# Kernel tuning notes

Hardware: AMD Instinct MI355X
Metric: run time of the kernel (lower is better)

Reference implementation:

```python
import jax, jax.numpy as jnp
import numpy as np

B, N, C = 128, 320, 768
H = 12
T = 64    # template tokens (8x8)
S = 256   # search tokens (16x16)


def setup_inputs() -> dict:
    key = jax.random.key(0)
    k1, k2, k3, k4 = jax.random.split(key, 4)
    return {
        "x1": jax.random.normal(k1, (B, N, C), dtype=jnp.float32),
        "x2": jax.random.normal(k2, (B, N, C), dtype=jnp.float32),
        "qkv_w": jax.random.normal(k3, (3 * C, C), dtype=jnp.float32) * 0.02,
        "proj_w": jax.random.normal(k4, (C, C), dtype=jnp.float32) * 0.02,
        "proj_b": jnp.zeros((C,), dtype=jnp.float32),
    }


def reference(x1, x2, qkv_w, proj_w, proj_b):
    # concat template tokens from x1 with search tokens from x2
    x = jnp.concatenate([x1[:, :T, :], x2[:, T:, :]], axis=1)  # [B, N, C]
    b, n, c = x.shape
    d = c // H
    scale = d ** -0.5

    qkv = (x @ qkv_w.T).reshape(b, n, 3, H, d).transpose(2, 0, 3, 1, 4)  # [3,B,H,N,D]
    q, k, v = qkv[0], qkv[1], qkv[2]

    # template -> template self-attention
    q_mt, k_mt, v_mt = q[:, :, :T], k[:, :, :T], v[:, :, :T]
    attn_mt = jax.nn.softmax(jnp.einsum('bhtd,bhsd->bhts', q_mt, k_mt) * scale, axis=-1)
    x_mt = jnp.einsum('bhts,bhsd->bhtd', attn_mt, v_mt).transpose(0, 2, 1, 3).reshape(b, T, c)

    # search -> all cross+self attention
    q_s = q[:, :, T:]
    attn_s = jax.nn.softmax(jnp.einsum('bhqd,bhkd->bhqk', q_s, k) * scale, axis=-1)
    x_s = jnp.einsum('bhqk,bhkd->bhqd', attn_s, v).transpose(0, 2, 1, 3).reshape(b, S, c)

    out = jnp.concatenate([x_mt, x_s], axis=1) @ proj_w.T + proj_b
    return out
```

## Files before the change

kernel.cpp:

```cpp
#include <hip/hip_runtime.h>
#include <hip/hip_bf16.h>
#include <stdint.h>

#define B_   128
#define N_   320
#define C_   768
#define H_   12
#define D_   64
#define NT_  (B_*N_)
#define K3_  (3*C_)
#define NKT  12
#define TE   (256*64)

typedef __attribute__((ext_vector_type(8))) __bf16 bf16x8;
typedef __attribute__((ext_vector_type(4))) float  f32x4;

__device__ __forceinline__ unsigned short f2bf(float f) {
  union { float f; unsigned u; } v; v.f = f;
  return (unsigned short)((v.u + 0x7fffu + ((v.u >> 16) & 1u)) >> 16);
}

__device__ __forceinline__ void gload16(const unsigned short* g, unsigned short* l) {
  __builtin_amdgcn_global_load_lds((const __attribute__((address_space(1))) void*)g,
                                   (__attribute__((address_space(3))) void*)l,
                                   16, 0, 0);
}

__global__ void prep_x(const float* __restrict__ x1, const float* __restrict__ x2,
                       unsigned short* __restrict__ xb) {
  const unsigned total4 = (unsigned)NT_ * C_ / 4;
  const unsigned stride = gridDim.x * blockDim.x;
  for (unsigned i = blockIdx.x * blockDim.x + threadIdx.x; i < total4; i += stride) {
    unsigned tok = i / (C_ / 4);
    unsigned n   = tok % N_;
    const float* src = (n < 64u) ? x1 : x2;
    float4 v = *(const float4*)(src + (size_t)i * 4u);
    ushort4 o;
    o.x = f2bf(v.x); o.y = f2bf(v.y); o.z = f2bf(v.z); o.w = f2bf(v.w);
    *(ushort4*)(xb + (size_t)i * 4u) = o;
  }
}

__global__ void prep_w(const float* __restrict__ qkv_w, const float* __restrict__ proj_w,
                       unsigned short* __restrict__ wq, unsigned short* __restrict__ wp) {
  const int QKV4 = (K3_ * C_) / 4;
  const int Q4   = (C_ * C_) / 4;
  const int P4   = (C_ * C_) / 4;
  int i = blockIdx.x * 256 + threadIdx.x;
  if (i < QKV4) {
    float s = (i < Q4) ? 0.125f : 1.0f;
    float4 v = *(const float4*)(qkv_w + (size_t)i * 4);
    ushort4 o;
    o.x = f2bf(v.x * s); o.y = f2bf(v.y * s); o.z = f2bf(v.z * s); o.w = f2bf(v.w * s);
    *(ushort4*)(wq + (size_t)i * 4) = o;
  } else if (i < QKV4 + P4) {
    int j = i - QKV4;
    float4 v = *(const float4*)(proj_w + (size_t)j * 4);
    ushort4 o;
    o.x = f2bf(v.x); o.y = f2bf(v.y); o.z = f2bf(v.z); o.w = f2bf(v.w);
    *(ushort4*)(wp + (size_t)j * 4) = o;
  }
}

__device__ __forceinline__ void stage_half(const unsigned short* __restrict__ g,
                                           int grow0, int kt,
                                           unsigned short* lds_tile, int half,
                                           int w, int lane) {
  const int r0 = half * 128 + w * 16;
  const int rr = lane >> 3;
  const int sp = (lane & 7) ^ rr;
#pragma unroll
  for (int i = 0; i < 2; i++) {
    const unsigned short* gp = g + (size_t)(grow0 + r0 + i * 8 + rr) * 768 + kt * 64 + sp * 8;
    unsigned short* lp = lds_tile + (r0 + i * 8) * 64;
    gload16(gp, lp);
  }
}

__device__ __forceinline__ bf16x8 lds_frag(const unsigned short* tile, int row, int pp) {
  const char* p = (const char*)tile + row * 128 + (((pp) ^ (row & 7)) * 16);
  return *(const bf16x8*)p;
}

__device__ __forceinline__ void gemm_kloop(const unsigned short* __restrict__ Ag,
                                           const unsigned short* __restrict__ Wg,
                                           int row0, int col0,
                                           unsigned short* As, unsigned short* Bs,
                                           f32x4 (&acc)[8][4]) {
  const int tid = threadIdx.x, lane = tid & 63, w = tid >> 6;
  const int wr = w >> 2, wc = w & 3;
  const int lr = lane & 15, kg = lane >> 4;

  stage_half(Ag, row0, 0, As, 0, w, lane);
  stage_half(Ag, row0, 0, As, 1, w, lane);
  stage_half(Wg, col0, 0, Bs, 0, w, lane);
  stage_half(Wg, col0, 0, Bs, 1, w, lane);
  stage_half(Wg, col0, 1, Bs + TE, 0, w, lane);
  stage_half(Wg, col0, 1, Bs + TE, 1, w, lane);
  asm volatile("s_waitcnt vmcnt(4)" ::: "memory");
  __builtin_amdgcn_s_barrier();
  asm volatile("" ::: "memory");

  bf16x8 bf_[2][4];
#pragma unroll 2
  for (int t = 0; t < NKT; ++t) {
    unsigned short* Ac = As + (t & 1) * TE;
    unsigned short* Bc = Bs + (t & 1) * TE;
#pragma unroll
    for (int q = 0; q < 4; ++q) {
      bf16x8 af_[2][2];
#pragma unroll
      for (int f = 0; f < 2; ++f)
#pragma unroll
        for (int ks = 0; ks < 2; ++ks)
          af_[f][ks] = lds_frag(Ac, wr * 128 + q * 32 + f * 16 + lr, ks * 4 + kg);
      if (q == 0) {
#pragma unroll
        for (int nf = 0; nf < 4; ++nf)
#pragma unroll
          for (int ks = 0; ks < 2; ++ks)
            bf_[ks][nf] = lds_frag(Bc, wc * 64 + nf * 16 + lr, ks * 4 + kg);
      }
      if (q == 0)      { if (t + 1 < NKT) stage_half(Ag, row0, t + 1, As + ((t + 1) & 1) * TE, 0, w, lane); }
      else if (q == 1) { if (t + 1 < NKT) stage_half(Ag, row0, t + 1, As + ((t + 1) & 1) * TE, 1, w, lane); }
      else if (q == 2) { if (t + 2 < NKT) stage_half(Wg, col0, t + 2, Bs + (t & 1) * TE, 0, w, lane); }
      else             { if (t + 2 < NKT) stage_half(Wg, col0, t + 2, Bs + (t & 1) * TE, 1, w, lane); }
      asm volatile("" ::: "memory");
      __builtin_amdgcn_s_barrier();
      asm volatile("" ::: "memory");
      __builtin_amdgcn_s_setprio(1);
#pragma unroll
      for (int f = 0; f < 2; ++f)
#pragma unroll
        for (int nf = 0; nf < 4; ++nf) {
          const int mf = q * 2 + f;
          acc[mf][nf] = __builtin_amdgcn_mfma_f32_16x16x32_bf16(af_[f][0], bf_[0][nf], acc[mf][nf], 0, 0, 0);
          acc[mf][nf] = __builtin_amdgcn_mfma_f32_16x16x32_bf16(af_[f][1], bf_[1][nf], acc[mf][nf], 0, 0, 0);
        }
      __builtin_amdgcn_s_setprio(0);
      asm volatile("" ::: "memory");
      if (q == 3) {
        if (t < NKT - 2)       asm volatile("s_waitcnt vmcnt(4)" ::: "memory");
        else if (t == NKT - 2) asm volatile("s_waitcnt vmcnt(0)" ::: "memory");
      }
      __builtin_amdgcn_s_barrier();
      asm volatile("" ::: "memory");
    }
  }
}

__global__ void __launch_bounds__(512, 2) gemm_qkv(const unsigned short* __restrict__ A,
                                                   const unsigned short* __restrict__ W,
                                                   unsigned short* __restrict__ qb,
                                                   unsigned short* __restrict__ kb,
                                                   unsigned short* __restrict__ vb) {
  __shared__ __align__(16) unsigned short As[2 * TE];
  __shared__ __align__(16) unsigned short Bs[2 * TE];
  const int tid = threadIdx.x, lane = tid & 63, w = tid >> 6;
  const int wr = w >> 2, wc = w & 3;
  const int lr = lane & 15, kg = lane >> 4;
  const int bid = blockIdx.x;
  const int wg = (bid & 7) * 180 + (bid >> 3);
  const int bm = wg / 9, bn = wg % 9;
  const int row0 = bm * 256, col0 = bn * 256;

  f32x4 acc[8][4] = {};
  gemm_kloop(A, W, row0, col0, As, Bs, acc);

  const int which = bn / 3;
  const int colq  = (bn % 3) * 256 + wc * 64;
  if (which == 2) {
#pragma unroll
    for (int mf = 0; mf < 8; ++mf) {
      const int m0 = row0 + wr * 128 + mf * 16 + kg * 4;
      const unsigned bq = (unsigned)m0 / 320u;
      const unsigned t0 = (unsigned)m0 - bq * 320u;
#pragma unroll
      for (int nf = 0; nf < 4; ++nf) {
        const int nn = colq + nf * 16 + lr;
        const int h = nn >> 6, dd = nn & 63;
        ushort4 o;
        o.x = f2bf(acc[mf][nf][0]); o.y = f2bf(acc[mf][nf][1]);
        o.z = f2bf(acc[mf][nf][2]); o.w = f2bf(acc[mf][nf][3]);
        *(ushort4*)&vb[(((int)bq * 12 + h) * 64 + dd) * 320 + (int)t0] = o;
      }
    }
  } else {
    unsigned short* dst = (which == 0) ? qb : kb;
#pragma unroll
    for (int mf = 0; mf < 8; ++mf) {
      const int m0 = row0 + wr * 128 + mf * 16 + kg * 4;
      const unsigned bq = (unsigned)m0 / 320u;
      const unsigned t0 = (unsigned)m0 - bq * 320u;
#pragma unroll
      for (int nf = 0; nf < 4; ++nf) {
        const int nn = colq + nf * 16 + lr;
        const int h = nn >> 6, dd = nn & 63;
        const int base = (((int)bq * 12 + h) * 320 + (int)t0) * 64 + dd;
#pragma unroll
        for (int r = 0; r < 4; r++)
          dst[base + r * 64] = f2bf(acc[mf][nf][r]);
      }
    }
  }
}

__global__ void __launch_bounds__(256) attn(const unsigned short* __restrict__ qb,
                                            const unsigned short* __restrict__ kb,
                                            const unsigned short* __restrict__ vb,
                                            unsigned short* __restrict__ ab) {
  __shared__ __align__(16) unsigned short Ks[64 * 64];
  __shared__ __align__(16) unsigned short Vt[64 * 64];
  __shared__ __align__(16) unsigned short Pl[4 * 16 * 64];
  const int bid = blockIdx.x;
  const int qt = bid % 5, bh = bid / 5;
  const int tid = threadIdx.x, lane = tid & 63, w = tid >> 6;
  const int lr = lane & 15, kg = lane >> 4;

  const int qrow = qt * 64 + w * 16 + lr;
  const unsigned short* qptr = qb + (bh * 320 + qrow) * 64;
  const bf16x8 qa0 = *(const bf16x8*)(qptr + kg * 8);
  const bf16x8 qa1 = *(const bf16x8*)(qptr + 32 + kg * 8);

  f32x4 o[4] = {};
  float mrun[4] = {-1e30f, -1e30f, -1e30f, -1e30f};
  float lrun[4] = {0.f, 0.f, 0.f, 0.f};
  const int nchunk = (qt == 0) ? 1 : 5;

  const int c0 = w, c1 = w + 4;
  const int srow0 = c0 * 8 + (lane >> 3);
  const int srow1 = c1 * 8 + (lane >> 3);
  const int slot  = lane & 7;
  const int part0 = slot ^ (srow0 & 7);
  const int part1 = slot ^ (srow1 & 7);
  const unsigned short* kbase = kb + bh * 320 * 64;
  const unsigned short* vbase = vb + bh * 64 * 320;
  unsigned short* lk0 = &Ks[c0 * 512];
  unsigned short* lk1 = &Ks[c1 * 512];
  unsigned short* lv0 = &Vt[c0 * 512];
  unsigned short* lv1 = &Vt[c1 * 512];
  char* PwB = (char*)&Pl[w * 1024];

  for (int kc = 0; kc < nchunk; kc++) {
    gload16(kbase + (kc * 64 + srow0) * 64 + part0 * 8, lk0);
    gload16(kbase + (kc * 64 + srow1) * 64 + part1 * 8, lk1);
    gload16(vbase + srow0 * 320 + kc * 64 + part0 * 8, lv0);
    gload16(vbase + srow1 * 320 + kc * 64 + part1 * 8, lv1);
    __syncthreads();

    f32x4 s[4];
#pragma unroll
    for (int kt = 0; kt < 4; kt++) {
      const int key = kt * 16 + lr;
      const char* kr = (const char*)Ks + key * 128;
      const unsigned sw = (unsigned)((key & 7) << 4);
      bf16x8 k0 = *(const bf16x8*)(kr + ((kg * 16) ^ sw));
      bf16x8 k1 = *(const bf16x8*)(kr + ((64 + kg * 16) ^ sw));
      f32x4 z = {0.f, 0.f, 0.f, 0.f};
      z = __builtin_amdgcn_mfma_f32_16x16x32_bf16(qa0, k0, z, 0, 0, 0);
      z = __builtin_amdgcn_mfma_f32_16x16x32_bf16(qa1, k1, z, 0, 0, 0);
      s[kt] = z;
    }

#pragma unroll
    for (int r = 0; r < 4; r++) {
      float rm = fmaxf(fmaxf(s[0][r], s[1][r]), fmaxf(s[2][r], s[3][r]));
      rm = fmaxf(rm, __shfl_xor(rm, 1));
      rm = fmaxf(rm, __shfl_xor(rm, 2));
      rm = fmaxf(rm, __shfl_xor(rm, 4));
      rm = fmaxf(rm, __shfl_xor(rm, 8));
      const float mn = fmaxf(mrun[r], rm);
      const float alpha = __expf(mrun[r] - mn);
      mrun[r] = mn;
      const int q = kg * 4 + r;
      char* prow = PwB + q * 128;
      const unsigned sw = (unsigned)((q & 7) << 4);
      float rs = 0.f;
#pragma unroll
      for (int kt = 0; kt < 4; kt++) {
        const float p = __expf(s[kt][r] - mn);
        rs += p;
        const int key = kt * 16 + lr;
        *(unsigned short*)(prow + ((key * 2) ^ sw)) = f2bf(p);
      }
      rs += __shfl_xor(rs, 1);
      rs += __shfl_xor(rs, 2);
      rs += __shfl_xor(rs, 4);
      rs += __shfl_xor(rs, 8);
      lrun[r] = lrun[r] * alpha + rs;
#pragma unroll
      for (int dt = 0; dt < 4; dt++) o[dt][r] *= alpha;
    }

    asm volatile("s_waitcnt lgkmcnt(0)" ::: "memory");

    {
      const char* par = (const char*)PwB + lr * 128;
      const unsigned swp = (unsigned)((lr & 7) << 4);
      bf16x8 p0 = *(const bf16x8*)(par + ((kg * 16) ^ swp));
      bf16x8 p1 = *(const bf16x8*)(par + ((64 + kg * 16) ^ swp));
#pragma unroll
      for (int dt = 0; dt < 4; dt++) {
        const int d = dt * 16 + lr;
        const char* vr = (const char*)Vt + d * 128;
        const unsigned swv = (unsigned)((d & 7) << 4);
        bf16x8 v0 = *(const bf16x8*)(vr + ((kg * 16) ^ swv));
        bf16x8 v1 = *(const bf16x8*)(vr + ((64 + kg * 16) ^ swv));
        o[dt] = __builtin_amdgcn_mfma_f32_16x16x32_bf16(p0, v0, o[dt], 0, 0, 0);
        o[dt] = __builtin_amdgcn_mfma_f32_16x16x32_bf16(p1, v1, o[dt], 0, 0, 0);
      }
    }
    __syncthreads();
  }

  const int b = bh / 12, h = bh - b * 12;
#pragma unroll
  for (int r = 0; r < 4; r++) {
    const float inv = 1.0f / lrun[r];
    const int token = b * 320 + qt * 64 + w * 16 + kg * 4 + r;
    unsigned short* orow = ab + token * 768 + h * 64;
#pragma unroll
    for (int dt = 0; dt < 4; dt++)
      orow[dt * 16 + lr] = f2bf(o[dt][r] * inv);
  }
}

__global__ void __launch_bounds__(512, 2) gemm_proj(const unsigned short* __restrict__ A,
                                                    const unsigned short* __restrict__ W,
                                                    const float* __restrict__ bias,
                                                    float* __restrict__ out) {
  __shared__ __align__(16) unsigned short As[2 * TE];
  __shared__ __align__(16) unsigned short Bs[2 * TE];
  const int tid = threadIdx.x, lane = tid & 63, w = tid >> 6;
  const int wr = w >> 2, wc = w & 3;
  const int lr = lane & 15, kg = lane >> 4;
  const int bid = blockIdx.x;
  const int wg = (bid & 7) * 60 + (bid >> 3);
  const int bm = wg / 3, bn = wg % 3;
  const int row0 = bm * 256, col0 = bn * 256;

  f32x4 acc[8][4] = {};
  gemm_kloop(A, W, row0, col0, As, Bs, acc);

#pragma unroll
  for (int nf = 0; nf < 4; ++nf) {
    const int nn = col0 + wc * 64 + nf * 16 + lr;
    const float bv = bias[nn];
#pragma unroll
    for (int mf = 0; mf < 8; ++mf) {
      const int m0 = row0 + wr * 128 + mf * 16 + kg * 4;
      float* po = out + (size_t)m0 * 768 + nn;
#pragma unroll
      for (int r = 0; r < 4; r++)
        po[(size_t)r * 768] = acc[mf][nf][r] + bv;
    }
  }
}

extern "C" void kernel_launch(void* const* d_in, const int* in_sizes, int n_in,
                              void* d_out, int out_size, void* d_ws, size_t ws_size,
                              hipStream_t stream) {
  (void)in_sizes; (void)n_in; (void)out_size; (void)ws_size;
  const float* x1     = (const float*)d_in[0];
  const float* x2     = (const float*)d_in[1];
  const float* qkv_w  = (const float*)d_in[2];
  const float* proj_w = (const float*)d_in[3];
  const float* proj_b = (const float*)d_in[4];
  float* out = (float*)d_out;

  const size_t TOK = (size_t)NT_ * C_;
  unsigned short* xb = (unsigned short*)d_ws;
  unsigned short* qb = xb + TOK;
  unsigned short* kb = qb + TOK;
  unsigned short* vb = kb + TOK;
  unsigned short* ab = vb + TOK;
  unsigned short* wq = ab + TOK;
  unsigned short* wp = wq + (size_t)K3_ * C_;

  prep_x<<<8192, 256, 0, stream>>>(x1, x2, xb);
  prep_w<<<2304, 256, 0, stream>>>(qkv_w, proj_w, wq, wp);
  gemm_qkv<<<160 * 9, 512, 0, stream>>>(xb, wq, qb, kb, vb);
  attn<<<1536 * 5, 256, 0, stream>>>(qb, kb, vb, ab);
  gemm_proj<<<160 * 3, 512, 0, stream>>>(ab, wp, proj_b, out);
}
```

Baseline: 409.9 us.

## Rewrite GEMM k-loop as macro-unrolled pipeline with precomputed LDS/global pointers

```diff
diff --git a/kernel.cpp b/kernel.cpp
--- a/kernel.cpp
+++ b/kernel.cpp
@@ -62,91 +62,93 @@
   }
 }
 
-__device__ __forceinline__ void stage_half(const unsigned short* __restrict__ g,
-                                           int grow0, int kt,
-                                           unsigned short* lds_tile, int half,
-                                           int w, int lane) {
-  const int r0 = half * 128 + w * 16;
-  const int rr = lane >> 3;
-  const int sp = (lane & 7) ^ rr;
-#pragma unroll
-  for (int i = 0; i < 2; i++) {
-    const unsigned short* gp = g + (size_t)(grow0 + r0 + i * 8 + rr) * 768 + kt * 64 + sp * 8;
-    unsigned short* lp = lds_tile + (r0 + i * 8) * 64;
-    gload16(gp, lp);
-  }
-}
-
-__device__ __forceinline__ bf16x8 lds_frag(const unsigned short* tile, int row, int pp) {
-  const char* p = (const char*)tile + row * 128 + (((pp) ^ (row & 7)) * 16);
-  return *(const bf16x8*)p;
-}
-
-__device__ __forceinline__ void gemm_kloop(const unsigned short* __restrict__ Ag,
-                                           const unsigned short* __restrict__ Wg,
-                                           int row0, int col0,
-                                           unsigned short* As, unsigned short* Bs,
-                                           f32x4 (&acc)[8][4]) {
+#define BARR do { asm volatile("" ::: "memory"); __builtin_amdgcn_s_barrier(); asm volatile("" ::: "memory"); } while(0)
+#define DSW  asm volatile("s_waitcnt lgkmcnt(0)" ::: "memory")
+#define VMW(n) asm volatile("s_waitcnt vmcnt(" #n ")" ::: "memory")
+#define NOPW do {} while(0)
+#define PRIO1 __builtin_amdgcn_s_setprio(1)
+#define PRIO0 __builtin_amdgcn_s_setprio(0)
+#define RD(base, off) (*(const bf16x8*)((base) + (off)))
+
+#define LDA_Q(QQ, PARX) do { \
+    a_[0][0] = RD(bAk0, (PARX)*32768 + (QQ)*8192);        \
+    a_[0][1] = RD(bAk1, (PARX)*32768 + (QQ)*8192);        \
+    a_[1][0] = RD(bAk0, (PARX)*32768 + (QQ)*8192 + 2048); \
+    a_[1][1] = RD(bAk1, (PARX)*32768 + (QQ)*8192 + 2048); } while(0)
+
+#define LDB(PARX) do { \
+    _Pragma("unroll") for (int nf = 0; nf < 4; ++nf) { \
+      b_[0][nf] = RD(bBk0, (PARX)*32768 + nf*2048); \
+      b_[1][nf] = RD(bBk1, (PARX)*32768 + nf*2048); } } while(0)
+
+#define MFMA_Q(QQ) do { \
+    _Pragma("unroll") for (int ks = 0; ks < 2; ++ks) \
+    _Pragma("unroll") for (int f = 0; f < 2; ++f) \
+    _Pragma("unroll") for (int nf = 0; nf < 4; ++nf) \
+      acc[(QQ)*2+f][nf] = __builtin_amdgcn_mfma_f32_16x16x32_bf16(a_[f][ks], b_[ks][nf], acc[(QQ)*2+f][nf], 0, 0, 0); \
+  } while(0)
+
+#define STGA_H0(PARX) do { gload16(gA00, dA + ((PARX)^1)*TE);        gload16(gA01, dA + ((PARX)^1)*TE + 512);  gA00 += 64; gA01 += 64; } while(0)
+#define STGA_H1(PARX) do { gload16(gA10, dA + ((PARX)^1)*TE + 8192); gload16(gA11, dA + ((PARX)^1)*TE + 8704); gA10 += 64; gA11 += 64; } while(0)
+#define STGB_H0(PARX) do { gload16(gB00, dB + (PARX)*TE);            gload16(gB01, dB + (PARX)*TE + 512);      gB00 += 64; gB01 += 64; } while(0)
+#define STGB_H1(PARX) do { gload16(gB10, dB + (PARX)*TE + 8192);     gload16(gB11, dB + (PARX)*TE + 8704);     gB10 += 64; gB11 += 64; } while(0)
+
+#define KTILE(PARX, SA_, SB_, W1_, W3_) do { \
+    LDA_Q(0, PARX); LDB(PARX); if (SA_) STGA_H0(PARX); \
+    BARR; DSW; PRIO1; MFMA_Q(0); PRIO0; BARR; \
+    LDA_Q(1, PARX); if (SA_) STGA_H1(PARX); \
+    BARR; DSW; PRIO1; MFMA_Q(1); PRIO0; W1_; BARR; \
+    LDA_Q(2, PARX); if (SB_) STGB_H0(PARX); \
+    BARR; DSW; PRIO1; MFMA_Q(2); PRIO0; BARR; \
+    LDA_Q(3, PARX); if (SB_) STGB_H1(PARX); \
+    BARR; DSW; PRIO1; MFMA_Q(3); PRIO0; W3_; BARR; \
+  } while(0)
+
+__device__ __forceinline__ void kloop256(const unsigned short* __restrict__ Ag,
+                                         const unsigned short* __restrict__ Wg,
+                                         int row0, int col0,
+                                         unsigned short* As, unsigned short* Bs,
+                                         f32x4 (&acc)[8][4]) {
   const int tid = threadIdx.x, lane = tid & 63, w = tid >> 6;
   const int wr = w >> 2, wc = w & 3;
   const int lr = lane & 15, kg = lane >> 4;
-
-  stage_half(Ag, row0, 0, As, 0, w, lane);
-  stage_half(Ag, row0, 0, As, 1, w, lane);
-  stage_half(Wg, col0, 0, Bs, 0, w, lane);
-  stage_half(Wg, col0, 0, Bs, 1, w, lane);
-  stage_half(Wg, col0, 1, Bs + TE, 0, w, lane);
-  stage_half(Wg, col0, 1, Bs + TE, 1, w, lane);
-  asm volatile("s_waitcnt vmcnt(4)" ::: "memory");
-  __builtin_amdgcn_s_barrier();
-  asm volatile("" ::: "memory");
-
-  bf16x8 bf_[2][4];
-#pragma unroll 2
-  for (int t = 0; t < NKT; ++t) {
-    unsigned short* Ac = As + (t & 1) * TE;
-    unsigned short* Bc = Bs + (t & 1) * TE;
-#pragma unroll
-    for (int q = 0; q < 4; ++q) {
-      bf16x8 af_[2][2];
-#pragma unroll
-      for (int f = 0; f < 2; ++f)
-#pragma unroll
-        for (int ks = 0; ks < 2; ++ks)
-          af_[f][ks] = lds_frag(Ac, wr * 128 + q * 32 + f * 16 + lr, ks * 4 + kg);
-      if (q == 0) {
-#pragma unroll
-        for (int nf = 0; nf < 4; ++nf)
-#pragma unroll
-          for (int ks = 0; ks < 2; ++ks)
-            bf_[ks][nf] = lds_frag(Bc, wc * 64 + nf * 16 + lr, ks * 4 + kg);
-      }
-      if (q == 0)      { if (t + 1 < NKT) stage_half(Ag, row0, t + 1, As + ((t + 1) & 1) * TE, 0, w, lane); }
-      else if (q == 1) { if (t + 1 < NKT) stage_half(Ag, row0, t + 1, As + ((t + 1) & 1) * TE, 1, w, lane); }
-      else if (q == 2) { if (t + 2 < NKT) stage_half(Wg, col0, t + 2, Bs + (t & 1) * TE, 0, w, lane); }
-      else             { if (t + 2 < NKT) stage_half(Wg, col0, t + 2, Bs + (t & 1) * TE, 1, w, lane); }
-      asm volatile("" ::: "memory");
-      __builtin_amdgcn_s_barrier();
-      asm volatile("" ::: "memory");
-      __builtin_amdgcn_s_setprio(1);
-#pragma unroll
-      for (int f = 0; f < 2; ++f)
-#pragma unroll
-        for (int nf = 0; nf < 4; ++nf) {
-          const int mf = q * 2 + f;
-          acc[mf][nf] = __builtin_amdgcn_mfma_f32_16x16x32_bf16(af_[f][0], bf_[0][nf], acc[mf][nf], 0, 0, 0);
-          acc[mf][nf] = __builtin_amdgcn_mfma_f32_16x16x32_bf16(af_[f][1], bf_[1][nf], acc[mf][nf], 0, 0, 0);
-        }
-      __builtin_amdgcn_s_setprio(0);
-      asm volatile("" ::: "memory");
-      if (q == 3) {
-        if (t < NKT - 2)       asm volatile("s_waitcnt vmcnt(4)" ::: "memory");
-        else if (t == NKT - 2) asm volatile("s_waitcnt vmcnt(0)" ::: "memory");
-      }
-      __builtin_amdgcn_s_barrier();
-      asm volatile("" ::: "memory");
-    }
-  }
+  const int rr = lane >> 3;
+  const int sp = (lane & 7) ^ rr;
+
+  const char* bAk0 = (const char*)As + wr*4096 + lr*128 + (((0*4)+kg) ^ (lr & 7))*16;
+  const char* bAk1 = (const char*)As + wr*4096 + lr*128 + (((1*4)+kg) ^ (lr & 7))*16;
+  const char* bBk0 = (const char*)Bs + wc*8192 + lr*128 + (((0*4)+kg) ^ (lr & 7))*16;
+  const char* bBk1 = (const char*)Bs + wc*8192 + lr*128 + (((1*4)+kg) ^ (lr & 7))*16;
+
+  const unsigned short* gA00 = Ag + (size_t)(row0 +   0 + w*16 + 0 + rr)*768 + 1*64 + sp*8;
+  const unsigned short* gA01 = Ag + (size_t)(row0 +   0 + w*16 + 8 + rr)*768 + 1*64 + sp*8;
+  const unsigned short* gA10 = Ag + (size_t)(row0 + 128 + w*16 + 0 + rr)*768 + 1*64 + sp*8;
+  const unsigned short* gA11 = Ag + (size_t)(row0 + 128 + w*16 + 8 + rr)*768 + 1*64 + sp*8;
+  const unsigned short* gB00 = Wg + (size_t)(col0 +   0 + w*16 + 0 + rr)*768 + 2*64 + sp*8;
+  const unsigned short* gB01 = Wg + (size_t)(col0 +   0 + w*16 + 8 + rr)*768 + 2*64 + sp*8;
+  const unsigned short* gB10 = Wg + (size_t)(col0 + 128 + w*16 + 0 + rr)*768 + 2*64 + sp*8;
+  const unsigned short* gB11 = Wg + (size_t)(col0 + 128 + w*16 + 8 + rr)*768 + 2*64 + sp*8;
+
+  unsigned short* dA = As + w*1024;
+  unsigned short* dB = Bs + w*1024;
+
+  gload16(gA00 - 64,  dA);              gload16(gA01 - 64,  dA + 512);
+  gload16(gA10 - 64,  dA + 8192);       gload16(gA11 - 64,  dA + 8704);
+  gload16(gB00 - 128, dB);              gload16(gB01 - 128, dB + 512);
+  gload16(gB10 - 128, dB + 8192);       gload16(gB11 - 128, dB + 8704);
+  gload16(gB00 - 64,  dB + TE);         gload16(gB01 - 64,  dB + TE + 512);
+  gload16(gB10 - 64,  dB + TE + 8192);  gload16(gB11 - 64,  dB + TE + 8704);
+  VMW(4);
+  BARR;
+
+  bf16x8 a_[2][2], b_[2][4];
+#pragma unroll 1
+  for (int tt = 0; tt < 5; ++tt) {
+    KTILE(0, 1, 1, VMW(8), VMW(6));
+    KTILE(1, 1, 1, VMW(8), VMW(6));
+  }
+  KTILE(0, 1, 0, VMW(8), VMW(2));
+  KTILE(1, 0, 0, VMW(0), NOPW);
 }
 
 __global__ void __launch_bounds__(512, 2) gemm_qkv(const unsigned short* __restrict__ A,
@@ -165,14 +167,14 @@
   const int row0 = bm * 256, col0 = bn * 256;
 
   f32x4 acc[8][4] = {};
-  gemm_kloop(A, W, row0, col0, As, Bs, acc);
+  kloop256(A, W, row0, col0, As, Bs, acc);
 
   const int which = bn / 3;
   const int colq  = (bn % 3) * 256 + wc * 64;
   if (which == 2) {
 #pragma unroll
     for (int mf = 0; mf < 8; ++mf) {
-      const int m0 = row0 + wr * 128 + mf * 16 + kg * 4;
+      const int m0 = row0 + (mf >> 1) * 64 + wr * 32 + (mf & 1) * 16 + kg * 4;
       const unsigned bq = (unsigned)m0 / 320u;
       const unsigned t0 = (unsigned)m0 - bq * 320u;
 #pragma unroll
@@ -189,7 +191,7 @@
     unsigned short* dst = (which == 0) ? qb : kb;
 #pragma unroll
     for (int mf = 0; mf < 8; ++mf) {
-      const int m0 = row0 + wr * 128 + mf * 16 + kg * 4;
+      const int m0 = row0 + (mf >> 1) * 64 + wr * 32 + (mf & 1) * 16 + kg * 4;
       const unsigned bq = (unsigned)m0 / 320u;
       const unsigned t0 = (unsigned)m0 - bq * 320u;
 #pragma unroll
@@ -340,7 +342,7 @@
   const int row0 = bm * 256, col0 = bn * 256;
 
   f32x4 acc[8][4] = {};
-  gemm_kloop(A, W, row0, col0, As, Bs, acc);
+  kloop256(A, W, row0, col0, As, Bs, acc);
 
 #pragma unroll
   for (int nf = 0; nf < 4; ++nf) {
@@ -348,7 +350,7 @@
     const float bv = bias[nn];
 #pragma unroll
     for (int mf = 0; mf < 8; ++mf) {
-      const int m0 = row0 + wr * 128 + mf * 16 + kg * 4;
+      const int m0 = row0 + (mf >> 1) * 64 + wr * 32 + (mf & 1) * 16 + kg * 4;
       float* po = out + (size_t)m0 * 768 + nn;
 #pragma unroll
       for (int r = 0; r < 4; r++)
```

Result: slower. 420.7 us (+2.6%).
